# Optimization experiments

Hardware: AMD Instinct MI355X
Metric: run time of the kernel (lower is better)

The kernel has to match this reference:

```python
import jax, jax.numpy as jnp
import numpy as np

B, T, E, HD = 8, 2048, 1024, 64  # batch, seq (== n_ctx), n_embd, head_dim = n_embd // n_head


def setup_inputs() -> dict:
    key = jax.random.key(0)
    k1, k2, k3, k4 = jax.random.split(key, 4)
    x = jax.random.normal(k1, (B, T, E), dtype=jnp.float32)
    s = E ** -0.5  # Linear-like init scale
    Wq = jax.random.normal(k2, (E, HD), dtype=jnp.float32) * s
    Wk = jax.random.normal(k3, (E, HD), dtype=jnp.float32) * s
    Wv = jax.random.normal(k4, (E, HD), dtype=jnp.float32) * s
    return {"x": x, "Wq": Wq, "Wk": Wk, "Wv": Wv}


def reference(x, Wq, Wk, Wv):
    # q,k,v: [B, T, HD]
    q = jnp.einsum('bte,eh->bth', x, Wq)
    k = jnp.einsum('bte,eh->bth', x, Wk)
    v = jnp.einsum('bte,eh->bth', x, Wv)
    scale = k.shape[-1] ** -0.5
    # scores: [B, T, T]
    alpha = jnp.einsum('bqh,bkh->bqk', q, k) * scale
    causal = jnp.tril(jnp.ones((T, T), dtype=bool))
    alpha = jnp.where(causal, alpha, -jnp.inf)
    alpha = jax.nn.softmax(alpha, axis=-1)
    # dropout with p=0.0 is identity in eval
    h = jnp.einsum('bqk,bkh->bqh', alpha, v)  # [B, T, HD]
    return h
```

## Files before the change

### kernel.cpp

```cpp
#include <hip/hip_runtime.h>
#include <hip/hip_bf16.h>
#include <math.h>

#define BATCH 8
#define T 2048
#define E 1024
#define HD 64
#define BT (BATCH * T)

typedef __bf16 bf16_t;
typedef bf16_t bf16x4 __attribute__((ext_vector_type(4)));
typedef bf16_t bf16x8 __attribute__((ext_vector_type(8)));
typedef float f32x4 __attribute__((ext_vector_type(4)));

#define MFMA(a, b, c) __builtin_amdgcn_mfma_f32_16x16x32_bf16((a), (b), (c), 0, 0, 0)

#define QSCALE (0.125f * 1.44269504088896340736f)


__global__ __launch_bounds__(256) void prep_w(const float* __restrict__ Wq,
                                              const float* __restrict__ Wk,
                                              const float* __restrict__ Wv,
                                              bf16_t* __restrict__ WTt) {
    const int nt  = blockIdx.x >> 3;
    const int kc0 = (blockIdx.x & 7) * 128;
    const int tid = threadIdx.x;
    const int l16 = tid & 15;
    const int k8  = (kc0 >> 3) + (tid >> 4);
    const int n   = nt * 16 + l16;
    const int m   = n >> 6;
    const int col = n & 63;
    const float* W = (m == 0) ? Wq : (m == 1) ? Wk : Wv;
    const float scale = (m == 0) ? QSCALE : 1.0f;
    bf16x8 o;
#pragma unroll
    for (int j = 0; j < 8; j++) {
        o[j] = (bf16_t)(W[(size_t)(k8 * 8 + j) * HD + col] * scale);
    }
    *reinterpret_cast<bf16x8*>(WTt + (size_t)nt * 16384 + k8 * 128 + l16 * 8) = o;
}

__global__ __launch_bounds__(256) void qkv_proj(
    const float* __restrict__ x,
    const bf16_t* __restrict__ WTt,
    bf16_t* __restrict__ qt,
    bf16_t* __restrict__ kt,
    bf16_t* __restrict__ vt)
{
    const int tid  = threadIdx.x;
    const int wave = tid >> 6;
    const int lane = tid & 63;
    const int l16  = lane & 15;
    const int quad = lane >> 4;
    const int wr   = wave >> 1;
    const int wc   = wave & 1;
    const int rowbase0 = blockIdx.x * 32;

    const float* xr = x + (size_t)(rowbase0 + wr * 16 + l16) * E + quad * 8;
    const bf16_t* Bb = WTt + (size_t)(wc * 6) * 16384 + lane * 8;

    f32x4 acc[6] = {};

    f32x4 xa0 = *reinterpret_cast<const f32x4*>(xr);
    f32x4 xb0 = *reinterpret_cast<const f32x4*>(xr + 4);
    f32x4 xa1 = *reinterpret_cast<const f32x4*>(xr + 32);
    f32x4 xb1 = *reinterpret_cast<const f32x4*>(xr + 36);
    bf16x8 bcur[2][6];
#pragma unroll
    for (int ks = 0; ks < 2; ks++) {
#pragma unroll
        for (int tc = 0; tc < 6; tc++) {
            bcur[ks][tc] = *reinterpret_cast<const bf16x8*>(
                Bb + (size_t)tc * 16384 + (ks * 32) * 16);
        }
    }

    for (int kc = 0; kc < E; kc += 64) {
        const int kn = (kc + 64) & (E - 1);
        const f32x4 nxa0 = *reinterpret_cast<const f32x4*>(xr + kn);
        const f32x4 nxb0 = *reinterpret_cast<const f32x4*>(xr + kn + 4);
        const f32x4 nxa1 = *reinterpret_cast<const f32x4*>(xr + kn + 32);
        const f32x4 nxb1 = *reinterpret_cast<const f32x4*>(xr + kn + 36);
        bf16x8 bn[2][6];
#pragma unroll
        for (int ks = 0; ks < 2; ks++) {
#pragma unroll
            for (int tc = 0; tc < 6; tc++) {
                bn[ks][tc] = *reinterpret_cast<const bf16x8*>(
                    Bb + (size_t)tc * 16384 + (kn + ks * 32) * 16);
            }
        }

        bf16x8 a0, a1;
#pragma unroll
        for (int u = 0; u < 4; u++) {
            a0[u]     = (bf16_t)xa0[u];
            a0[4 + u] = (bf16_t)xb0[u];
            a1[u]     = (bf16_t)xa1[u];
            a1[4 + u] = (bf16_t)xb1[u];
        }

#pragma unroll
        for (int tc = 0; tc < 6; tc++) acc[tc] = MFMA(a0, bcur[0][tc], acc[tc]);
#pragma unroll
        for (int tc = 0; tc < 6; tc++) acc[tc] = MFMA(a1, bcur[1][tc], acc[tc]);

        xa0 = nxa0; xb0 = nxb0; xa1 = nxa1; xb1 = nxb1;
#pragma unroll
        for (int ks = 0; ks < 2; ks++) {
#pragma unroll
            for (int tc = 0; tc < 6; tc++) bcur[ks][tc] = bn[ks][tc];
        }
    }

    const int rowbase = rowbase0 + wr * 16;
#pragma unroll
    for (int tc = 0; tc < 6; tc++) {
        const int n0  = wc * 96 + tc * 16;
        const int m   = n0 >> 6;
        const int tcg = (n0 & 63) >> 4;
        if (m < 2) {
            bf16_t* dst = (m == 0) ? qt : kt;
            const size_t o0 = (size_t)(rowbase >> 4) * 1024 +
                              (size_t)(tcg * 2 + (l16 >> 3)) * 128 + (l16 & 7);
#pragma unroll
            for (int r = 0; r < 4; r++) {
                dst[o0 + (quad * 4 + r) * 8] = (bf16_t)acc[tc][r];
            }
        } else {
            const int b_    = rowbase >> 11;
            const int tbase = rowbase & (T - 1);
            const size_t o0 = (size_t)b_ * 131072 +
                              (size_t)((tbase >> 3) + (quad >> 1)) * 128 +
                              l16 * 8 + (quad & 1) * 4 + (size_t)tcg * 32768;
            bf16x4 pv;
#pragma unroll
            for (int r = 0; r < 4; r++) pv[r] = (bf16_t)acc[tc][r];
            *reinterpret_cast<bf16x4*>(vt + o0) = pv;
        }
    }
}

__global__ __launch_bounds__(512) void attn(
    const bf16_t* __restrict__ qtl,
    const bf16_t* __restrict__ ktl,
    const bf16_t* __restrict__ vtl,
    float* __restrict__ out)
{
    __shared__ __align__(16) bf16_t plds[8][16][40];
    __shared__ float opart[8][16][66];
    __shared__ float lpart[8][16];

    const int wave = threadIdx.x >> 6;
    const int lane = threadIdx.x & 63;
    const int l16  = lane & 15;
    const int quad = lane >> 4;
    const int group = wave >> 2;
    const int kw    = wave & 3;

    const int b  = blockIdx.x >> 6;
    const int pr = blockIdx.x & 63;
    const int qt = group ? (127 - pr) : pr;
    const int rowbase = qt * 16;

    const bf16_t* Qb = qtl + (size_t)((b * T + rowbase) >> 4) * 1024 + lane * 8;
    const bf16_t* Kb = ktl + (size_t)b * T * 64 + lane * 8;
    const bf16_t* Vb = vtl + (size_t)b * 131072 + lane * 8;

    const bf16x8 qf0 = *reinterpret_cast<const bf16x8*>(Qb);
    const bf16x8 qf1 = *reinterpret_cast<const bf16x8*>(Qb + 512);

    f32x4 o[4] = {};
    f32x4 lrun = {};

    const int nch = (rowbase + 47) >> 5;

    int k0 = kw * 32;
    bf16x8 kfa0 = *reinterpret_cast<const bf16x8*>(Kb + k0 * 64);
    bf16x8 kfb0 = *reinterpret_cast<const bf16x8*>(Kb + k0 * 64 + 512);
    bf16x8 kfa1 = *reinterpret_cast<const bf16x8*>(Kb + k0 * 64 + 1024);
    bf16x8 kfb1 = *reinterpret_cast<const bf16x8*>(Kb + k0 * 64 + 1536);
    bf16x8 vf0 = *reinterpret_cast<const bf16x8*>(Vb + k0 * 16);
    bf16x8 vf1 = *reinterpret_cast<const bf16x8*>(Vb + k0 * 16 + 32768);
    bf16x8 vf2 = *reinterpret_cast<const bf16x8*>(Vb + k0 * 16 + 65536);
    bf16x8 vf3 = *reinterpret_cast<const bf16x8*>(Vb + k0 * 16 + 98304);

    for (int c = kw; c < nch; c += 4) {
        k0 = c * 32;
        const int cn = (c + 4 < nch) ? (c + 4) : c;
        const int kn = cn * 32;
        bf16x8 nkfa0 = *reinterpret_cast<const bf16x8*>(Kb + kn * 64);
        bf16x8 nkfb0 = *reinterpret_cast<const bf16x8*>(Kb + kn * 64 + 512);
        bf16x8 nkfa1 = *reinterpret_cast<const bf16x8*>(Kb + kn * 64 + 1024);
        bf16x8 nkfb1 = *reinterpret_cast<const bf16x8*>(Kb + kn * 64 + 1536);
        bf16x8 nvf0 = *reinterpret_cast<const bf16x8*>(Vb + kn * 16);
        bf16x8 nvf1 = *reinterpret_cast<const bf16x8*>(Vb + kn * 16 + 32768);
        bf16x8 nvf2 = *reinterpret_cast<const bf16x8*>(Vb + kn * 16 + 65536);
        bf16x8 nvf3 = *reinterpret_cast<const bf16x8*>(Vb + kn * 16 + 98304);

        f32x4 s_lo = {};
        f32x4 s_hi = {};
        s_lo = MFMA(qf0, kfa0, s_lo);
        s_lo = MFMA(qf1, kfb0, s_lo);
        s_hi = MFMA(qf0, kfa1, s_hi);
        s_hi = MFMA(qf1, kfb1, s_hi);

        if (k0 + 31 > rowbase) {
            const int row = rowbase + quad * 4;
#pragma unroll
            for (int r = 0; r < 4; r++) {
                if (k0 + l16 > row + r)      s_lo[r] = -INFINITY;
                if (k0 + 16 + l16 > row + r) s_hi[r] = -INFINITY;
            }
        }

#pragma unroll
        for (int r = 0; r < 4; r++) {
            const float p0 = exp2f(s_lo[r]);
            const float p1 = exp2f(s_hi[r]);
            lrun[r] += p0 + p1;
            plds[wave][quad * 4 + r][l16]      = (bf16_t)p0;
            plds[wave][quad * 4 + r][16 + l16] = (bf16_t)p1;
        }
        const bf16x8 pf = *reinterpret_cast<const bf16x8*>(&plds[wave][l16][quad * 8]);

        o[0] = MFMA(pf, vf0, o[0]);
        o[1] = MFMA(pf, vf1, o[1]);
        o[2] = MFMA(pf, vf2, o[2]);
        o[3] = MFMA(pf, vf3, o[3]);

        kfa0 = nkfa0; kfb0 = nkfb0; kfa1 = nkfa1; kfb1 = nkfb1;
        vf0 = nvf0; vf1 = nvf1; vf2 = nvf2; vf3 = nvf3;
    }

#pragma unroll
    for (int r = 0; r < 4; r++) {
        float l = lrun[r];
        l += __shfl_xor(l, 1);
        l += __shfl_xor(l, 2);
        l += __shfl_xor(l, 4);
        l += __shfl_xor(l, 8);
        if (l16 == 0) lpart[wave][quad * 4 + r] = l;
#pragma unroll
        for (int nb = 0; nb < 4; nb++) {
            opart[wave][quad * 4 + r][nb * 16 + l16] = o[nb][r];
        }
    }
    __syncthreads();

    const int g    = threadIdx.x >> 8;
    const int gtid = threadIdx.x & 255;
    const int qtg  = g ? (127 - pr) : pr;
    const size_t outbase = (size_t)b * T + qtg * 16;
#pragma unroll
    for (int pass = 0; pass < 4; pass++) {
        const int row = pass * 4 + (gtid >> 6);
        const int col = gtid & 63;
        float osum = 0.f, lsum = 0.f;
#pragma unroll
        for (int w = 0; w < 4; w++) {
            osum += opart[g * 4 + w][row][col];
            lsum += lpart[g * 4 + w][row];
        }
        out[(outbase + row) * HD + col] = osum / lsum;
    }
}

extern "C" void kernel_launch(void* const* d_in, const int* in_sizes, int n_in,
                              void* d_out, int out_size, void* d_ws, size_t ws_size,
                              hipStream_t stream) {
    const float* x  = (const float*)d_in[0];
    const float* Wq = (const float*)d_in[1];
    const float* Wk = (const float*)d_in[2];
    const float* Wv = (const float*)d_in[3];
    float* out = (float*)d_out;

    bf16_t* ws  = (bf16_t*)d_ws;
    bf16_t* WTt = ws;
    bf16_t* qtl = WTt + (size_t)192 * E;
    bf16_t* ktl = qtl + (size_t)BT * HD;
    bf16_t* vtl = ktl + (size_t)BT * HD;

    prep_w<<<96, 256, 0, stream>>>(Wq, Wk, Wv, WTt);
    qkv_proj<<<512, 256, 0, stream>>>(x, WTt, qtl, ktl, vtl);
    attn<<<512, 512, 0, stream>>>(qtl, ktl, vtl, out);
}
```

Before: 144.2 us.

## Share x tile through LDS in QKV projection and double grid size

The QKV projection now handles 16 rows per block instead of 32. Each x element is loaded once from global memory and converted to bf16 once, then staged in a double-buffered LDS tile that all four waves read. Before, two waves each loaded and converted the same x rows. Each wave now covers 48 output columns instead of 96, and the grid doubles to 1024 blocks. Launch bounds occupancy hints are added to both the projection and attention kernels. In exchange, every k-step gets a block barrier, and the weight tiles are re-read by twice as many blocks.

```diff
diff --git a/kernel.cpp b/kernel.cpp
--- a/kernel.cpp
+++ b/kernel.cpp
@@ -40,83 +40,88 @@
     *reinterpret_cast<bf16x8*>(WTt + (size_t)nt * 16384 + k8 * 128 + l16 * 8) = o;
 }
 
-__global__ __launch_bounds__(256) void qkv_proj(
+__global__ __launch_bounds__(256, 4) void qkv_proj(
     const float* __restrict__ x,
     const bf16_t* __restrict__ WTt,
     bf16_t* __restrict__ qt,
     bf16_t* __restrict__ kt,
     bf16_t* __restrict__ vt)
 {
+    __shared__ __align__(16) bf16_t xbuf[2][16][72];
+
     const int tid  = threadIdx.x;
     const int wave = tid >> 6;
     const int lane = tid & 63;
     const int l16  = lane & 15;
     const int quad = lane >> 4;
-    const int wr   = wave >> 1;
-    const int wc   = wave & 1;
-    const int rowbase0 = blockIdx.x * 32;
-
-    const float* xr = x + (size_t)(rowbase0 + wr * 16 + l16) * E + quad * 8;
-    const bf16_t* Bb = WTt + (size_t)(wc * 6) * 16384 + lane * 8;
-
-    f32x4 acc[6] = {};
-
-    f32x4 xa0 = *reinterpret_cast<const f32x4*>(xr);
-    f32x4 xb0 = *reinterpret_cast<const f32x4*>(xr + 4);
-    f32x4 xa1 = *reinterpret_cast<const f32x4*>(xr + 32);
-    f32x4 xb1 = *reinterpret_cast<const f32x4*>(xr + 36);
-    bf16x8 bcur[2][6];
+    const int rowbase0 = blockIdx.x * 16;
+
+    const int srow = tid >> 4;
+    const int sseg = tid & 15;
+    const float* xsrc = x + (size_t)(rowbase0 + srow) * E + sseg * 4;
+
+    const bf16_t* Bb = WTt + (size_t)(wave * 3) * 16384 + lane * 8;
+
+    f32x4 acc[3] = {};
+
+    {
+        const f32x4 xa = *reinterpret_cast<const f32x4*>(xsrc);
+        bf16x4 xw;
+#pragma unroll
+        for (int u = 0; u < 4; u++) xw[u] = (bf16_t)xa[u];
+        *reinterpret_cast<bf16x4*>(&xbuf[0][srow][sseg * 4]) = xw;
+    }
+    bf16x8 bcur[2][3];
 #pragma unroll
     for (int ks = 0; ks < 2; ks++) {
 #pragma unroll
-        for (int tc = 0; tc < 6; tc++) {
+        for (int tc = 0; tc < 3; tc++) {
             bcur[ks][tc] = *reinterpret_cast<const bf16x8*>(
                 Bb + (size_t)tc * 16384 + (ks * 32) * 16);
         }
     }
-
+    __syncthreads();
+
+    int p = 0;
     for (int kc = 0; kc < E; kc += 64) {
         const int kn = (kc + 64) & (E - 1);
-        const f32x4 nxa0 = *reinterpret_cast<const f32x4*>(xr + kn);
-        const f32x4 nxb0 = *reinterpret_cast<const f32x4*>(xr + kn + 4);
-        const f32x4 nxa1 = *reinterpret_cast<const f32x4*>(xr + kn + 32);
-        const f32x4 nxb1 = *reinterpret_cast<const f32x4*>(xr + kn + 36);
-        bf16x8 bn[2][6];
+        const f32x4 nxa = *reinterpret_cast<const f32x4*>(xsrc + kn);
+        bf16x8 bn[2][3];
 #pragma unroll
         for (int ks = 0; ks < 2; ks++) {
 #pragma unroll
-            for (int tc = 0; tc < 6; tc++) {
+            for (int tc = 0; tc < 3; tc++) {
                 bn[ks][tc] = *reinterpret_cast<const bf16x8*>(
                     Bb + (size_t)tc * 16384 + (kn + ks * 32) * 16);
             }
         }
 
-        bf16x8 a0, a1;
-#pragma unroll
-        for (int u = 0; u < 4; u++) {
-            a0[u]     = (bf16_t)xa0[u];
-            a0[4 + u] = (bf16_t)xb0[u];
-            a1[u]     = (bf16_t)xa1[u];
-            a1[4 + u] = (bf16_t)xb1[u];
-        }
-
-#pragma unroll
-        for (int tc = 0; tc < 6; tc++) acc[tc] = MFMA(a0, bcur[0][tc], acc[tc]);
-#pragma unroll
-        for (int tc = 0; tc < 6; tc++) acc[tc] = MFMA(a1, bcur[1][tc], acc[tc]);
-
-        xa0 = nxa0; xb0 = nxb0; xa1 = nxa1; xb1 = nxb1;
+        const bf16x8 a0 = *reinterpret_cast<const bf16x8*>(&xbuf[p][l16][quad * 8]);
+        const bf16x8 a1 = *reinterpret_cast<const bf16x8*>(&xbuf[p][l16][32 + quad * 8]);
+
+#pragma unroll
+        for (int tc = 0; tc < 3; tc++) acc[tc] = MFMA(a0, bcur[0][tc], acc[tc]);
+#pragma unroll
+        for (int tc = 0; tc < 3; tc++) acc[tc] = MFMA(a1, bcur[1][tc], acc[tc]);
+
+        bf16x4 xw;
+#pragma unroll
+        for (int u = 0; u < 4; u++) xw[u] = (bf16_t)nxa[u];
+        *reinterpret_cast<bf16x4*>(&xbuf[p ^ 1][srow][sseg * 4]) = xw;
+        __syncthreads();
+        p ^= 1;
+
 #pragma unroll
         for (int ks = 0; ks < 2; ks++) {
 #pragma unroll
-            for (int tc = 0; tc < 6; tc++) bcur[ks][tc] = bn[ks][tc];
-        }
-    }
-
-    const int rowbase = rowbase0 + wr * 16;
-#pragma unroll
-    for (int tc = 0; tc < 6; tc++) {
-        const int n0  = wc * 96 + tc * 16;
+            for (int tc = 0; tc < 3; tc++) bcur[ks][tc] = bn[ks][tc];
+        }
+    }
+
+    const int rowbase = rowbase0;
+#pragma unroll
+    for (int tc = 0; tc < 3; tc++) {
+        const int n0  = wave * 48 + tc * 16;
         const int m   = n0 >> 6;
         const int tcg = (n0 & 63) >> 4;
         if (m < 2) {
@@ -141,7 +146,7 @@
     }
 }
 
-__global__ __launch_bounds__(512) void attn(
+__global__ __launch_bounds__(512, 2) void attn(
     const bf16_t* __restrict__ qtl,
     const bf16_t* __restrict__ ktl,
     const bf16_t* __restrict__ vtl,
@@ -282,6 +287,6 @@
     bf16_t* vtl = ktl + (size_t)BT * HD;
 
     prep_w<<<96, 256, 0, stream>>>(Wq, Wk, Wv, WTt);
-    qkv_proj<<<512, 256, 0, stream>>>(x, WTt, qtl, ktl, vtl);
+    qkv_proj<<<1024, 256, 0, stream>>>(x, WTt, qtl, ktl, vtl);
     attn<<<512, 512, 0, stream>>>(qtl, ktl, vtl, out);
 }
```

Result: faster. 132.7 us (-8.0%).
